# Kernel optimization log

Measured on AMD Instinct MI355X. Metric: run time of the kernel, lower is better.

## Reference

```python
import jax, jax.numpy as jnp
import numpy as np

B, LQ, LK = 4, 1024, 2048
DQ, DK, DV, D = 1024, 512, 512, 1024
H = 16
HD = D // H
EPS = 1e-5


def setup_inputs() -> dict:
    key = jax.random.key(0)
    ks = jax.random.split(key, 12)
    s = lambda fan: 1.0 / np.sqrt(fan)
    return {
        "query": jax.random.normal(ks[0], (B, LQ, DQ), jnp.float32),
        "key": jax.random.normal(ks[1], (B, LK, DK), jnp.float32),
        "value": jax.random.normal(ks[2], (B, LK, DV), jnp.float32),
        "key_padding_mask": jnp.ones((B, LK), jnp.int32),
        "Wq": jax.random.normal(ks[3], (DQ, D), jnp.float32) * s(DQ),
        "bq": jnp.zeros((D,), jnp.float32),
        "Wk": jax.random.normal(ks[4], (DK, D), jnp.float32) * s(DK),
        "bk": jnp.zeros((D,), jnp.float32),
        "Wv": jax.random.normal(ks[5], (DV, D), jnp.float32) * s(DV),
        "bv": jnp.zeros((D,), jnp.float32),
        "Wo": jax.random.normal(ks[6], (D, D), jnp.float32) * s(D),
        "bo": jnp.zeros((D,), jnp.float32),
        "ln_g": jnp.ones((D,), jnp.float32),
        "ln_b": jnp.zeros((D,), jnp.float32),
    }


def _layer_norm(x, g, b):
    mu = jnp.mean(x, axis=-1, keepdims=True)
    var = jnp.mean(jnp.square(x - mu), axis=-1, keepdims=True)
    return (x - mu) * jax.lax.rsqrt(var + EPS) * g + b


def reference(query, key, value, key_padding_mask, Wq, bq, Wk, bk, Wv, bv, Wo, bo, ln_g, ln_b):
    residual = query
    qn = _layer_norm(query, ln_g, ln_b)
    # projections -> [B, L, H, HD]
    q = (qn @ Wq + bq).reshape(B, LQ, H, HD)
    k = (key @ Wk + bk).reshape(B, LK, H, HD)
    v = (value @ Wv + bv).reshape(B, LK, H, HD)
    scale = HD ** -0.5
    # scores [B, H, Lq, Lk]
    scores = jnp.einsum("bqhd,bkhd->bhqk", q, k) * scale
    mask = (key_padding_mask != 0)[:, None, None, :]  # True = keep
    scores = jnp.where(mask, scores, -jnp.inf)
    attn = jax.nn.softmax(scores, axis=-1)
    # dropout is identity in eval mode
    ctx = jnp.einsum("bhqk,bkhd->bqhd", attn, v).reshape(B, LQ, D)
    out = ctx @ Wo + bo
    return out + residual
```

## Files before the change

### kernel.cpp

```cpp
#include <hip/hip_runtime.h>
#include <hip/hip_bf16.h>
#include <stdint.h>

#define Bn 4
#define LQ 1024
#define LK 2048
#define Dm 1024
#define Hn 16
#define HD 64

typedef __attribute__((ext_vector_type(4))) float f32x4;
typedef __attribute__((ext_vector_type(16))) float f32x16;
typedef __attribute__((ext_vector_type(8))) short bf16x8;

__device__ __forceinline__ ushort f2bf(float f) {
  union { float f; uint32_t u; } v; v.f = f;
  uint32_t r = v.u + 0x7FFF + ((v.u >> 16) & 1);
  return (ushort)(r >> 16);
}

__device__ __forceinline__ uint32_t cvt_pk_bf16(float lo, float hi) {
  uint32_t r;
  asm("v_cvt_pk_bf16_f32 %0, %1, %2" : "=v"(r) : "v"(lo), "v"(hi));
  return r;
}

__device__ __forceinline__ float exp2v(float x) {
  float r;
  asm("v_exp_f32 %0, %1" : "=v"(r) : "v"(x));
  return r;
}

__device__ __forceinline__ void gload16(const void* g, void* lds) {
  __builtin_amdgcn_global_load_lds(
      (const __attribute__((address_space(1))) void*)g,
      (__attribute__((address_space(3))) void*)lds, 16, 0, 0);
}

__device__ __forceinline__ void wait_vm0_barrier() {
  asm volatile("s_waitcnt vmcnt(0)" ::: "memory");
  __builtin_amdgcn_s_barrier();
}

__device__ __forceinline__ void wait_all_barrier() {
  asm volatile("s_waitcnt vmcnt(0) lgkmcnt(0)" ::: "memory");
  __builtin_amdgcn_s_barrier();
}

__global__ __launch_bounds__(256) void transpose_cast_kernel(
    const float* __restrict__ W, ushort* __restrict__ Wt, int K, int N) {
  __shared__ float tile[64][65];
  int k0 = blockIdx.x * 64, n0 = blockIdx.y * 64;
  int tx = threadIdx.x & 63, ty = threadIdx.x >> 6;
#pragma unroll
  for (int i = 0; i < 16; ++i) {
    int r = ty + i * 4;
    tile[r][tx] = W[(size_t)(k0 + r) * N + n0 + tx];
  }
  __syncthreads();
#pragma unroll
  for (int i = 0; i < 16; ++i) {
    int r = ty + i * 4;
    Wt[(size_t)(n0 + r) * K + k0 + tx] = f2bf(tile[tx][r]);
  }
}

__global__ __launch_bounds__(256) void cast_bf16_kernel(
    const float4* __restrict__ in, ushort4* __restrict__ out, int n4) {
  int i = blockIdx.x * blockDim.x + threadIdx.x;
  int stride = gridDim.x * blockDim.x;
  for (; i < n4; i += stride) {
    float4 v = in[i];
    out[i] = make_ushort4(f2bf(v.x), f2bf(v.y), f2bf(v.z), f2bf(v.w));
  }
}

__global__ __launch_bounds__(256) void ln_kernel(
    const float* __restrict__ x, const float* __restrict__ g,
    const float* __restrict__ b, ushort* __restrict__ y) {
  int row = blockIdx.x;
  const float4* xr = (const float4*)(x + (size_t)row * 1024);
  float4 v = xr[threadIdx.x];
  float s1 = v.x + v.y + v.z + v.w;
  float s2 = v.x * v.x + v.y * v.y + v.z * v.z + v.w * v.w;
#pragma unroll
  for (int off = 32; off > 0; off >>= 1) {
    s1 += __shfl_down(s1, off);
    s2 += __shfl_down(s2, off);
  }
  __shared__ float r1[4], r2[4];
  int w = threadIdx.x >> 6, lane = threadIdx.x & 63;
  if (lane == 0) { r1[w] = s1; r2[w] = s2; }
  __syncthreads();
  s1 = r1[0] + r1[1] + r1[2] + r1[3];
  s2 = r2[0] + r2[1] + r2[2] + r2[3];
  float mu = s1 * (1.0f / 1024.0f);
  float var = s2 * (1.0f / 1024.0f) - mu * mu;
  float rstd = rsqrtf(var + 1e-5f);
  float4 gv = ((const float4*)g)[threadIdx.x];
  float4 bv = ((const float4*)b)[threadIdx.x];
  ushort4 o;
  o.x = f2bf((v.x - mu) * rstd * gv.x + bv.x);
  o.y = f2bf((v.y - mu) * rstd * gv.y + bv.y);
  o.z = f2bf((v.z - mu) * rstd * gv.z + bv.z);
  o.w = f2bf((v.w - mu) * rstd * gv.w + bv.w);
  ((ushort4*)(y + (size_t)row * 1024))[threadIdx.x] = o;
}

__global__ __launch_bounds__(256) void qkv_gemm_kernel(
    const ushort* __restrict__ qn, const ushort* __restrict__ WqT,
    const float* __restrict__ bq, ushort* __restrict__ Qb,
    const ushort* __restrict__ keyb, const ushort* __restrict__ WkT,
    const float* __restrict__ bk, ushort* __restrict__ Kb,
    const ushort* __restrict__ valb, const ushort* __restrict__ WvT,
    const float* __restrict__ bv, ushort* __restrict__ Vt, float qscale) {
  __shared__ ushort As[2][128 * 64];
  __shared__ ushort Bs[2][128 * 64];

  int o = blockIdx.x;
  int logical = (o & 7) * 160 + (o >> 3);
  const ushort* A; const ushort* Bt; const float* bias; ushort* out;
  int M, K, bx, by, epi; float osc = 1.0f;
  if (logical < 256) {
    A = qn; Bt = WqT; bias = bq; out = Qb; M = 4096; K = 1024; epi = 0;
    osc = qscale; bx = logical & 7; by = logical >> 3;
  } else if (logical < 768) {
    int i = logical - 256;
    A = keyb; Bt = WkT; bias = bk; out = Kb; M = 8192; K = 512; epi = 0;
    bx = i & 7; by = i >> 3;
  } else {
    int i = logical - 768;
    A = valb; Bt = WvT; bias = bv; out = Vt; M = 8192; K = 512; epi = 1;
    bx = i & 7; by = i >> 3;
  }
  const int N = 1024;
  const int m0 = by * 128, n0 = bx * 128;

  const int t = threadIdx.x;
  const int lane = t & 63;
  const int w = t >> 6;
  const int wm = w >> 1, wn = w & 1;
  const int l31 = lane & 31, hl = lane >> 5;

  f32x16 acc[2][2] = {};

  const ushort* Ap[4];
  const ushort* Bp[4];
#pragma unroll
  for (int i = 0; i < 4; ++i) {
    int c = t + i * 256;
    int r = c >> 3, x = ((c & 7) ^ (r & 7)) * 8;
    Ap[i] = A + (size_t)(m0 + r) * K + x;
    Bp[i] = Bt + (size_t)(n0 + r) * K + x;
  }

  auto stage = [&](int buf, int kt) {
#pragma unroll
    for (int i = 0; i < 4; ++i) {
      gload16(Ap[i] + kt, (char*)As[buf] + (t + i * 256) * 16);
      gload16(Bp[i] + kt, (char*)Bs[buf] + (t + i * 256) * 16);
    }
  };

  stage(0, 0);
  wait_vm0_barrier();

  int cur = 0;
  for (int kt = 0; kt < K; kt += 64) {
    if (kt + 64 < K) stage(cur ^ 1, kt + 64);
    bf16x8 af[2][4], bfr[2][4];
#pragma unroll
    for (int m = 0; m < 2; ++m) {
      int row = wm * 64 + m * 32 + l31;
      const char* ar = (const char*)As[cur] + row * 128;
      int rs = row & 7;
#pragma unroll
      for (int kc = 0; kc < 4; ++kc)
        af[m][kc] = *(const bf16x8*)(ar + ((kc * 2 + hl) ^ rs) * 16);
    }
#pragma unroll
    for (int n = 0; n < 2; ++n) {
      int row = wn * 64 + n * 32 + l31;
      const char* br = (const char*)Bs[cur] + row * 128;
      int rs = row & 7;
#pragma unroll
      for (int kc = 0; kc < 4; ++kc)
        bfr[n][kc] = *(const bf16x8*)(br + ((kc * 2 + hl) ^ rs) * 16);
    }
#pragma unroll
    for (int kc = 0; kc < 4; ++kc)
#pragma unroll
      for (int m = 0; m < 2; ++m)
#pragma unroll
        for (int n = 0; n < 2; ++n)
          acc[m][n] = __builtin_amdgcn_mfma_f32_32x32x16_bf16(af[m][kc], bfr[n][kc], acc[m][n], 0, 0, 0);
    wait_vm0_barrier();
    cur ^= 1;
  }

  float bias_v[2];
#pragma unroll
  for (int n = 0; n < 2; ++n) bias_v[n] = bias[n0 + wn * 64 + n * 32 + l31];

#pragma unroll
  for (int m = 0; m < 2; ++m) {
    int rbase = m0 + wm * 64 + m * 32 + hl * 4;
#pragma unroll
    for (int n = 0; n < 2; ++n) {
      int col = n0 + wn * 64 + n * 32 + l31;
#pragma unroll
      for (int rq = 0; rq < 4; ++rq) {
        int row0 = rbase + rq * 8;
        if (epi == 1) {
          int bb = row0 >> 11;
          int key = row0 & 2047;
          int h = col >> 6, hd = col & 63;
          ushort4 pk;
          pk.x = f2bf(acc[m][n][rq * 4 + 0] + bias_v[n]);
          pk.y = f2bf(acc[m][n][rq * 4 + 1] + bias_v[n]);
          pk.z = f2bf(acc[m][n][rq * 4 + 2] + bias_v[n]);
          pk.w = f2bf(acc[m][n][rq * 4 + 3] + bias_v[n]);
          *(ushort4*)(out + ((size_t)((bb * 16 + h) * 64 + hd)) * 2048 + key) = pk;
        } else {
#pragma unroll
          for (int j = 0; j < 4; ++j) {
            int row = row0 + j;
            float v = (acc[m][n][rq * 4 + j] + bias_v[n]) * osc;
            out[(size_t)row * N + col] = f2bf(v);
          }
        }
      }
    }
  }
}

__global__ __launch_bounds__(256) void oproj_gemm_kernel(
    const ushort* __restrict__ A, const ushort* __restrict__ Bt,
    const float* __restrict__ bias, float* __restrict__ Cout,
    const float* __restrict__ residual, int M, int N, int K) {
  __shared__ ushort As[2][128 * 64];
  __shared__ ushort Bs[2][128 * 64];
  const int t = threadIdx.x;
  const int lane = t & 63;
  const int w = t >> 6;
  const int wm = w >> 1, wn = w & 1;
  const int m0 = blockIdx.y * 128, n0 = blockIdx.x * 128;
  const int l31 = lane & 31, hl = lane >> 5;

  f32x16 acc[2][2] = {};

  const ushort* Ap[4];
  const ushort* Bp[4];
#pragma unroll
  for (int i = 0; i < 4; ++i) {
    int c = t + i * 256;
    int r = c >> 3, x = ((c & 7) ^ (r & 7)) * 8;
    Ap[i] = A + (size_t)(m0 + r) * K + x;
    Bp[i] = Bt + (size_t)(n0 + r) * K + x;
  }

  auto stage = [&](int buf, int kt) {
#pragma unroll
    for (int i = 0; i < 4; ++i) {
      gload16(Ap[i] + kt, (char*)As[buf] + (t + i * 256) * 16);
      gload16(Bp[i] + kt, (char*)Bs[buf] + (t + i * 256) * 16);
    }
  };

  stage(0, 0);
  wait_vm0_barrier();

  int cur = 0;
  for (int kt = 0; kt < K; kt += 64) {
    if (kt + 64 < K) stage(cur ^ 1, kt + 64);
    bf16x8 af[2][4], bfr[2][4];
#pragma unroll
    for (int m = 0; m < 2; ++m) {
      int row = wm * 64 + m * 32 + l31;
      const char* ar = (const char*)As[cur] + row * 128;
      int rs = row & 7;
#pragma unroll
      for (int kc = 0; kc < 4; ++kc)
        af[m][kc] = *(const bf16x8*)(ar + ((kc * 2 + hl) ^ rs) * 16);
    }
#pragma unroll
    for (int n = 0; n < 2; ++n) {
      int row = wn * 64 + n * 32 + l31;
      const char* br = (const char*)Bs[cur] + row * 128;
      int rs = row & 7;
#pragma unroll
      for (int kc = 0; kc < 4; ++kc)
        bfr[n][kc] = *(const bf16x8*)(br + ((kc * 2 + hl) ^ rs) * 16);
    }
#pragma unroll
    for (int kc = 0; kc < 4; ++kc)
#pragma unroll
      for (int m = 0; m < 2; ++m)
#pragma unroll
        for (int n = 0; n < 2; ++n)
          acc[m][n] = __builtin_amdgcn_mfma_f32_32x32x16_bf16(af[m][kc], bfr[n][kc], acc[m][n], 0, 0, 0);
    wait_vm0_barrier();
    cur ^= 1;
  }

  float bias_v[2];
#pragma unroll
  for (int n = 0; n < 2; ++n) bias_v[n] = bias[n0 + wn * 64 + n * 32 + l31];

#pragma unroll
  for (int m = 0; m < 2; ++m) {
    int rbase = m0 + wm * 64 + m * 32 + hl * 4;
#pragma unroll
    for (int n = 0; n < 2; ++n) {
      int col = n0 + wn * 64 + n * 32 + l31;
#pragma unroll
      for (int rq = 0; rq < 4; ++rq) {
        int row0 = rbase + rq * 8;
#pragma unroll
        for (int j = 0; j < 4; ++j) {
          size_t idx = (size_t)(row0 + j) * N + col;
          Cout[idx] = acc[m][n][rq * 4 + j] + bias_v[n] + residual[idx];
        }
      }
    }
  }
}

__global__ __launch_bounds__(256) void attn_kernel(
    const ushort* __restrict__ Qb, const ushort* __restrict__ Kb,
    const ushort* __restrict__ Vt, const int* __restrict__ mask,
    ushort* __restrict__ ctx) {
  __shared__ __align__(16) char smem[128 + 2 * 16384];
  int* tilevalid = (int*)smem;
  char* KsBase = smem + 128;
  char* VsBase = smem + 128 + 16384;

  const int t = threadIdx.x, lane = t & 63, w = t >> 6;
  const int l31 = lane & 31, hl = lane >> 5;
  int o = blockIdx.x;
  int logical = (o & 7) * 64 + (o >> 3);
  const int b = logical >> 7;
  const int hh = (logical >> 3) & 15;
  const int q0 = (logical & 7) * 128;
  const int* maskp = mask + b * 2048;

  const int cA = t, cB = t + 256;
  const int rA = cA >> 3, rB = cB >> 3;
  const int xA = ((cA & 7) ^ (rA & 7)) * 8, xB = ((cB & 7) ^ (rB & 7)) * 8;
  const ushort* kpA = Kb + ((size_t)(b * 2048 + rA)) * 1024 + hh * 64 + xA;
  const ushort* kpB = Kb + ((size_t)(b * 2048 + rB)) * 1024 + hh * 64 + xB;
  const ushort* vpA = Vt + ((size_t)((b * 16 + hh) * 64 + rA)) * 2048 + xA;
  const ushort* vpB = Vt + ((size_t)((b * 16 + hh) * 64 + rB)) * 2048 + xB;

  auto stageKV = [&](int buf) {
    char* kd = KsBase + buf * 8192;
    char* vd = VsBase + buf * 8192;
    gload16(kpA, kd + cA * 16);
    gload16(kpB, kd + cB * 16);
    gload16(vpA, vd + cA * 16);
    gload16(vpB, vd + cB * 16);
  };

  if (t < 32) tilevalid[t] = 1;
  __syncthreads();
  stageKV(0);
  {
    const int* mp = maskp + t * 8;
    int ok = 1;
#pragma unroll
    for (int j = 0; j < 8; ++j) ok &= (mp[j] != 0) ? 1 : 0;
    atomicAnd(&tilevalid[t >> 3], ok);
  }

  bf16x8 qf[4];
  {
    int qrow = q0 + w * 32 + l31;
    const ushort* qp = Qb + ((size_t)(b * 1024 + qrow)) * 1024 + hh * 64 + hl * 8;
    qf[0] = *(const bf16x8*)(qp);
    qf[1] = *(const bf16x8*)(qp + 16);
    qf[2] = *(const bf16x8*)(qp + 32);
    qf[3] = *(const bf16x8*)(qp + 48);
  }

  const int rs = l31 & 7;
  int lo[2][2][4];
#pragma unroll
  for (int bu = 0; bu < 2; ++bu)
#pragma unroll
    for (int r2 = 0; r2 < 2; ++r2)
#pragma unroll
      for (int kc = 0; kc < 4; ++kc)
        lo[bu][r2][kc] = 128 + bu * 8192 + (r2 * 32 + l31) * 128 + (((kc * 2 + hl) ^ rs) * 16);

  f32x16 o_acc[2] = {};
  float m_run = -1e30f, l_run = 0.0f;

  wait_all_barrier();

  auto body = [&](const int CUR, int TILE) __attribute__((always_inline)) {
    if (TILE + 1 < 32) {
      kpA += 64 * 1024; kpB += 64 * 1024; vpA += 64; vpB += 64;
      stageKV(CUR ^ 1);
    }

    f32x16 sacc[2] = {};
    __builtin_amdgcn_s_setprio(1);
#pragma unroll
    for (int kb = 0; kb < 2; ++kb)
#pragma unroll
      for (int kc = 0; kc < 4; ++kc) {
        bf16x8 kf = *(const bf16x8*)(smem + lo[CUR][kb][kc]);
        sacc[kb] = __builtin_amdgcn_mfma_f32_32x32x16_bf16(kf, qf[kc], sacc[kb], 0, 0, 0);
      }
    __builtin_amdgcn_s_setprio(0);

    int allv = __builtin_amdgcn_readfirstlane(tilevalid[TILE]);
    if (!allv) {
      const int* mrow = maskp + TILE * 64 + 4 * hl;
#pragma unroll
      for (int kb = 0; kb < 2; ++kb)
#pragma unroll
        for (int rq = 0; rq < 4; ++rq) {
          int4 mv = *(const int4*)(mrow + kb * 32 + rq * 8);
          sacc[kb][rq * 4 + 0] = mv.x ? sacc[kb][rq * 4 + 0] : -1e30f;
          sacc[kb][rq * 4 + 1] = mv.y ? sacc[kb][rq * 4 + 1] : -1e30f;
          sacc[kb][rq * 4 + 2] = mv.z ? sacc[kb][rq * 4 + 2] : -1e30f;
          sacc[kb][rq * 4 + 3] = mv.w ? sacc[kb][rq * 4 + 3] : -1e30f;
        }
    }

    float tm = fmaxf(sacc[0][0], sacc[0][1]);
#pragma unroll
    for (int r = 2; r < 16; r += 2) tm = fmaxf(fmaxf(tm, sacc[0][r]), sacc[0][r + 1]);
#pragma unroll
    for (int r = 0; r < 16; r += 2) tm = fmaxf(fmaxf(tm, sacc[1][r]), sacc[1][r + 1]);
    {
      float s1 = tm, s2 = tm;
      asm("v_permlane32_swap_b32 %0, %1" : "+v"(s1), "+v"(s2));
      tm = fmaxf(tm, hl ? s1 : s2);
    }

    if (__any(tm - m_run > 11.5f)) {
      float mn = fmaxf(m_run, tm);
      float al = exp2v(m_run - mn);
      m_run = mn;
      l_run *= al;
#pragma unroll
      for (int df = 0; df < 2; ++df)
#pragma unroll
        for (int r = 0; r < 16; ++r) o_acc[df][r] *= al;
    }

    float psA = 0.0f, psB = 0.0f;
    uint32_t cpk[2][8];
#pragma unroll
    for (int kb = 0; kb < 2; ++kb)
#pragma unroll
      for (int rr = 0; rr < 8; ++rr) {
        float pa = exp2v(sacc[kb][2 * rr] - m_run);
        float pb = exp2v(sacc[kb][2 * rr + 1] - m_run);
        psA += pa; psB += pb;
        cpk[kb][rr] = cvt_pk_bf16(pa, pb);
      }
    float psum = psA + psB;
    {
      float s1 = psum, s2 = psum;
      asm("v_permlane32_swap_b32 %0, %1" : "+v"(s1), "+v"(s2));
      psum += hl ? s1 : s2;
    }
    l_run += psum;

    __builtin_amdgcn_s_setprio(1);
#pragma unroll
    for (int ks = 0; ks < 4; ++ks) {
      const int kb = ks >> 1, ci = (ks & 1) * 4;
      uint32_t a0 = cpk[kb][ci],     b0 = cpk[kb][ci + 2];
      uint32_t a1 = cpk[kb][ci + 1], b1 = cpk[kb][ci + 3];
      asm("v_permlane32_swap_b32 %0, %1" : "+v"(a0), "+v"(b0));
      asm("v_permlane32_swap_b32 %0, %1" : "+v"(a1), "+v"(b1));
      union { uint32_t u[4]; bf16x8 v; } pb_;
      pb_.u[0] = a0; pb_.u[1] = a1; pb_.u[2] = b0; pb_.u[3] = b1;
#pragma unroll
      for (int df = 0; df < 2; ++df) {
        bf16x8 vf = *(const bf16x8*)(smem + lo[CUR][df][ks] + 16384);
        o_acc[df] = __builtin_amdgcn_mfma_f32_32x32x16_bf16(vf, pb_.v, o_acc[df], 0, 0, 0);
      }
    }
    __builtin_amdgcn_s_setprio(0);

    wait_vm0_barrier();
  };

  for (int tile = 0; tile < 32; tile += 2) {
    body(0, tile);
    body(1, tile + 1);
  }

  float inv = l_run > 0.0f ? 1.0f / l_run : 0.0f;
  char* ob = KsBase + w * 4096;
#pragma unroll
  for (int df = 0; df < 2; ++df)
#pragma unroll
    for (int rq = 0; rq < 4; ++rq) {
      ushort4 pk;
      pk.x = f2bf(o_acc[df][rq * 4 + 0] * inv);
      pk.y = f2bf(o_acc[df][rq * 4 + 1] * inv);
      pk.z = f2bf(o_acc[df][rq * 4 + 2] * inv);
      pk.w = f2bf(o_acc[df][rq * 4 + 3] * inv);
      *(ushort4*)(ob + l31 * 128 + (((df * 4 + rq) ^ (l31 & 7)) * 16) + hl * 8) = pk;
    }
  asm volatile("s_waitcnt lgkmcnt(0)" ::: "memory");
#pragma unroll
  for (int i = 0; i < 4; ++i) {
    int q = (lane >> 3) + i * 8;
    int ch = lane & 7;
    uint4 v = *(const uint4*)(ob + q * 128 + ((ch ^ (q & 7)) * 16));
    int qrow = q0 + w * 32 + q;
    *(uint4*)(ctx + ((size_t)(b * 1024 + qrow)) * 1024 + hh * 64 + ch * 8) = v;
  }
}

extern "C" void kernel_launch(void* const* d_in, const int* in_sizes, int n_in,
                              void* d_out, int out_size, void* d_ws, size_t ws_size,
                              hipStream_t stream) {
  const float* query = (const float*)d_in[0];
  const float* key   = (const float*)d_in[1];
  const float* value = (const float*)d_in[2];
  const int*   mask  = (const int*)d_in[3];
  const float* Wq = (const float*)d_in[4];
  const float* bq = (const float*)d_in[5];
  const float* Wk = (const float*)d_in[6];
  const float* bk = (const float*)d_in[7];
  const float* Wv = (const float*)d_in[8];
  const float* bv = (const float*)d_in[9];
  const float* Wo = (const float*)d_in[10];
  const float* bo = (const float*)d_in[11];
  const float* ln_g = (const float*)d_in[12];
  const float* ln_b = (const float*)d_in[13];
  float* out = (float*)d_out;

  char* p = (char*)d_ws;
  auto alloc = [&](size_t elems) { ushort* r = (ushort*)p; p += elems * 2; return r; };
  ushort* WqT  = alloc((size_t)1024 * 1024);
  ushort* WkT  = alloc((size_t)1024 * 512);
  ushort* WvT  = alloc((size_t)1024 * 512);
  ushort* WoT  = alloc((size_t)1024 * 1024);
  ushort* qn   = alloc((size_t)4096 * 1024);
  ushort* keyb = alloc((size_t)8192 * 512);
  ushort* valb = alloc((size_t)8192 * 512);
  ushort* Qb   = alloc((size_t)4096 * 1024);
  ushort* Kb   = alloc((size_t)8192 * 1024);
  ushort* Vt   = alloc((size_t)8192 * 1024);
  ushort* ctx  = alloc((size_t)4096 * 1024);
  (void)ws_size; (void)in_sizes; (void)n_in; (void)out_size;

  const float QSCALE = 0.125f * 1.44269504f;

  dim3 blk(256);
  transpose_cast_kernel<<<dim3(16, 16), blk, 0, stream>>>(Wq, WqT, 1024, 1024);
  transpose_cast_kernel<<<dim3(8, 16),  blk, 0, stream>>>(Wk, WkT, 512, 1024);
  transpose_cast_kernel<<<dim3(8, 16),  blk, 0, stream>>>(Wv, WvT, 512, 1024);
  transpose_cast_kernel<<<dim3(16, 16), blk, 0, stream>>>(Wo, WoT, 1024, 1024);
  cast_bf16_kernel<<<dim3(1024), blk, 0, stream>>>((const float4*)key,   (ushort4*)keyb, (8192 * 512) / 4);
  cast_bf16_kernel<<<dim3(1024), blk, 0, stream>>>((const float4*)value, (ushort4*)valb, (8192 * 512) / 4);
  ln_kernel<<<dim3(4096), blk, 0, stream>>>(query, ln_g, ln_b, qn);

  qkv_gemm_kernel<<<dim3(1280), blk, 0, stream>>>(
      qn, WqT, bq, Qb, keyb, WkT, bk, Kb, valb, WvT, bv, Vt, QSCALE);

  attn_kernel<<<dim3(512), blk, 0, stream>>>(Qb, Kb, Vt, mask, ctx);

  oproj_gemm_kernel<<<dim3(8, 32), blk, 0, stream>>>(ctx, WoT, bo, out, query, 4096, 1024, 1024);
}
```

Measured before the change: 165.9 us.

## Use 8 waves per GEMM block and overlap next-tile loads with compute

Both the QKV and output-projection GEMM kernels move from 4 to 8 waves per 128x128 tile, so each wave computes a 64x32 sub-tile with half the accumulators and half the global loads per thread. The K loop now issues the next stage's loads and waits only for the previous stage (vmcnt(4)) before the barrier. The end-of-iteration barrier waits only on LDS reads. The aim is more latency hiding through extra waves and overlap of memory with MFMA work. In exchange, the A fragments are read from LDS by twice as many waves.

```diff
diff --git a/kernel.cpp b/kernel.cpp
--- a/kernel.cpp
+++ b/kernel.cpp
@@ -44,6 +44,11 @@
 
 __device__ __forceinline__ void wait_all_barrier() {
   asm volatile("s_waitcnt vmcnt(0) lgkmcnt(0)" ::: "memory");
+  __builtin_amdgcn_s_barrier();
+}
+
+__device__ __forceinline__ void wait_lgkm0_barrier() {
+  asm volatile("s_waitcnt lgkmcnt(0)" ::: "memory");
   __builtin_amdgcn_s_barrier();
 }
 
@@ -107,7 +112,7 @@
   ((ushort4*)(y + (size_t)row * 1024))[threadIdx.x] = o;
 }
 
-__global__ __launch_bounds__(256) void qkv_gemm_kernel(
+__global__ __launch_bounds__(512) void qkv_gemm_kernel(
     const ushort* __restrict__ qn, const ushort* __restrict__ WqT,
     const float* __restrict__ bq, ushort* __restrict__ Qb,
     const ushort* __restrict__ keyb, const ushort* __restrict__ WkT,
@@ -120,17 +125,17 @@
   int o = blockIdx.x;
   int logical = (o & 7) * 160 + (o >> 3);
   const ushort* A; const ushort* Bt; const float* bias; ushort* out;
-  int M, K, bx, by, epi; float osc = 1.0f;
+  int K, bx, by, epi; float osc = 1.0f;
   if (logical < 256) {
-    A = qn; Bt = WqT; bias = bq; out = Qb; M = 4096; K = 1024; epi = 0;
+    A = qn; Bt = WqT; bias = bq; out = Qb; K = 1024; epi = 0;
     osc = qscale; bx = logical & 7; by = logical >> 3;
   } else if (logical < 768) {
     int i = logical - 256;
-    A = keyb; Bt = WkT; bias = bk; out = Kb; M = 8192; K = 512; epi = 0;
+    A = keyb; Bt = WkT; bias = bk; out = Kb; K = 512; epi = 0;
     bx = i & 7; by = i >> 3;
   } else {
     int i = logical - 768;
-    A = valb; Bt = WvT; bias = bv; out = Vt; M = 8192; K = 512; epi = 1;
+    A = valb; Bt = WvT; bias = bv; out = Vt; K = 512; epi = 1;
     bx = i & 7; by = i >> 3;
   }
   const int N = 1024;
@@ -139,36 +144,41 @@
   const int t = threadIdx.x;
   const int lane = t & 63;
   const int w = t >> 6;
-  const int wm = w >> 1, wn = w & 1;
+  const int wm = w >> 2, wn = w & 3;
   const int l31 = lane & 31, hl = lane >> 5;
 
-  f32x16 acc[2][2] = {};
-
-  const ushort* Ap[4];
-  const ushort* Bp[4];
-#pragma unroll
-  for (int i = 0; i < 4; ++i) {
-    int c = t + i * 256;
+  f32x16 acc[2] = {};
+
+  const ushort* Ap[2];
+  const ushort* Bp[2];
+#pragma unroll
+  for (int i = 0; i < 2; ++i) {
+    int c = t + i * 512;
     int r = c >> 3, x = ((c & 7) ^ (r & 7)) * 8;
     Ap[i] = A + (size_t)(m0 + r) * K + x;
     Bp[i] = Bt + (size_t)(n0 + r) * K + x;
   }
 
   auto stage = [&](int buf, int kt) {
-#pragma unroll
-    for (int i = 0; i < 4; ++i) {
-      gload16(Ap[i] + kt, (char*)As[buf] + (t + i * 256) * 16);
-      gload16(Bp[i] + kt, (char*)Bs[buf] + (t + i * 256) * 16);
-    }
+    gload16(Ap[0] + kt, (char*)As[buf] + (size_t)t * 16);
+    gload16(Ap[1] + kt, (char*)As[buf] + (size_t)(t + 512) * 16);
+    gload16(Bp[0] + kt, (char*)Bs[buf] + (size_t)t * 16);
+    gload16(Bp[1] + kt, (char*)Bs[buf] + (size_t)(t + 512) * 16);
   };
 
   stage(0, 0);
-  wait_vm0_barrier();
 
   int cur = 0;
   for (int kt = 0; kt < K; kt += 64) {
-    if (kt + 64 < K) stage(cur ^ 1, kt + 64);
-    bf16x8 af[2][4], bfr[2][4];
+    if (kt + 64 < K) {
+      stage(cur ^ 1, kt + 64);
+      asm volatile("s_waitcnt vmcnt(4)" ::: "memory");
+    } else {
+      asm volatile("s_waitcnt vmcnt(0)" ::: "memory");
+    }
+    __builtin_amdgcn_s_barrier();
+
+    bf16x8 af[2][4], bfr[4];
 #pragma unroll
     for (int m = 0; m < 2; ++m) {
       int row = wm * 64 + m * 32 + l31;
@@ -178,63 +188,56 @@
       for (int kc = 0; kc < 4; ++kc)
         af[m][kc] = *(const bf16x8*)(ar + ((kc * 2 + hl) ^ rs) * 16);
     }
-#pragma unroll
-    for (int n = 0; n < 2; ++n) {
-      int row = wn * 64 + n * 32 + l31;
+    {
+      int row = wn * 32 + l31;
       const char* br = (const char*)Bs[cur] + row * 128;
       int rs = row & 7;
 #pragma unroll
       for (int kc = 0; kc < 4; ++kc)
-        bfr[n][kc] = *(const bf16x8*)(br + ((kc * 2 + hl) ^ rs) * 16);
+        bfr[kc] = *(const bf16x8*)(br + ((kc * 2 + hl) ^ rs) * 16);
     }
 #pragma unroll
     for (int kc = 0; kc < 4; ++kc)
 #pragma unroll
       for (int m = 0; m < 2; ++m)
-#pragma unroll
-        for (int n = 0; n < 2; ++n)
-          acc[m][n] = __builtin_amdgcn_mfma_f32_32x32x16_bf16(af[m][kc], bfr[n][kc], acc[m][n], 0, 0, 0);
-    wait_vm0_barrier();
+        acc[m] = __builtin_amdgcn_mfma_f32_32x32x16_bf16(af[m][kc], bfr[kc], acc[m], 0, 0, 0);
+
+    wait_lgkm0_barrier();
     cur ^= 1;
   }
 
-  float bias_v[2];
-#pragma unroll
-  for (int n = 0; n < 2; ++n) bias_v[n] = bias[n0 + wn * 64 + n * 32 + l31];
+  const int col = n0 + wn * 32 + l31;
+  const float bias_v = bias[col];
 
 #pragma unroll
   for (int m = 0; m < 2; ++m) {
     int rbase = m0 + wm * 64 + m * 32 + hl * 4;
 #pragma unroll
-    for (int n = 0; n < 2; ++n) {
-      int col = n0 + wn * 64 + n * 32 + l31;
-#pragma unroll
-      for (int rq = 0; rq < 4; ++rq) {
-        int row0 = rbase + rq * 8;
-        if (epi == 1) {
-          int bb = row0 >> 11;
-          int key = row0 & 2047;
-          int h = col >> 6, hd = col & 63;
-          ushort4 pk;
-          pk.x = f2bf(acc[m][n][rq * 4 + 0] + bias_v[n]);
-          pk.y = f2bf(acc[m][n][rq * 4 + 1] + bias_v[n]);
-          pk.z = f2bf(acc[m][n][rq * 4 + 2] + bias_v[n]);
-          pk.w = f2bf(acc[m][n][rq * 4 + 3] + bias_v[n]);
-          *(ushort4*)(out + ((size_t)((bb * 16 + h) * 64 + hd)) * 2048 + key) = pk;
-        } else {
-#pragma unroll
-          for (int j = 0; j < 4; ++j) {
-            int row = row0 + j;
-            float v = (acc[m][n][rq * 4 + j] + bias_v[n]) * osc;
-            out[(size_t)row * N + col] = f2bf(v);
-          }
+    for (int rq = 0; rq < 4; ++rq) {
+      int row0 = rbase + rq * 8;
+      if (epi == 1) {
+        int bb = row0 >> 11;
+        int key = row0 & 2047;
+        int h = col >> 6, hd = col & 63;
+        ushort4 pk;
+        pk.x = f2bf(acc[m][rq * 4 + 0] + bias_v);
+        pk.y = f2bf(acc[m][rq * 4 + 1] + bias_v);
+        pk.z = f2bf(acc[m][rq * 4 + 2] + bias_v);
+        pk.w = f2bf(acc[m][rq * 4 + 3] + bias_v);
+        *(ushort4*)(out + ((size_t)((bb * 16 + h) * 64 + hd)) * 2048 + key) = pk;
+      } else {
+#pragma unroll
+        for (int j = 0; j < 4; ++j) {
+          int row = row0 + j;
+          float v = (acc[m][rq * 4 + j] + bias_v) * osc;
+          out[(size_t)row * N + col] = f2bf(v);
         }
       }
     }
   }
 }
 
-__global__ __launch_bounds__(256) void oproj_gemm_kernel(
+__global__ __launch_bounds__(512) void oproj_gemm_kernel(
     const ushort* __restrict__ A, const ushort* __restrict__ Bt,
     const float* __restrict__ bias, float* __restrict__ Cout,
     const float* __restrict__ residual, int M, int N, int K) {
@@ -243,37 +246,42 @@
   const int t = threadIdx.x;
   const int lane = t & 63;
   const int w = t >> 6;
-  const int wm = w >> 1, wn = w & 1;
+  const int wm = w >> 2, wn = w & 3;
   const int m0 = blockIdx.y * 128, n0 = blockIdx.x * 128;
   const int l31 = lane & 31, hl = lane >> 5;
 
-  f32x16 acc[2][2] = {};
-
-  const ushort* Ap[4];
-  const ushort* Bp[4];
-#pragma unroll
-  for (int i = 0; i < 4; ++i) {
-    int c = t + i * 256;
+  f32x16 acc[2] = {};
+
+  const ushort* Ap[2];
+  const ushort* Bp[2];
+#pragma unroll
+  for (int i = 0; i < 2; ++i) {
+    int c = t + i * 512;
     int r = c >> 3, x = ((c & 7) ^ (r & 7)) * 8;
     Ap[i] = A + (size_t)(m0 + r) * K + x;
     Bp[i] = Bt + (size_t)(n0 + r) * K + x;
   }
 
   auto stage = [&](int buf, int kt) {
-#pragma unroll
-    for (int i = 0; i < 4; ++i) {
-      gload16(Ap[i] + kt, (char*)As[buf] + (t + i * 256) * 16);
-      gload16(Bp[i] + kt, (char*)Bs[buf] + (t + i * 256) * 16);
-    }
+    gload16(Ap[0] + kt, (char*)As[buf] + (size_t)t * 16);
+    gload16(Ap[1] + kt, (char*)As[buf] + (size_t)(t + 512) * 16);
+    gload16(Bp[0] + kt, (char*)Bs[buf] + (size_t)t * 16);
+    gload16(Bp[1] + kt, (char*)Bs[buf] + (size_t)(t + 512) * 16);
   };
 
   stage(0, 0);
-  wait_vm0_barrier();
 
   int cur = 0;
   for (int kt = 0; kt < K; kt += 64) {
-    if (kt + 64 < K) stage(cur ^ 1, kt + 64);
-    bf16x8 af[2][4], bfr[2][4];
+    if (kt + 64 < K) {
+      stage(cur ^ 1, kt + 64);
+      asm volatile("s_waitcnt vmcnt(4)" ::: "memory");
+    } else {
+      asm volatile("s_waitcnt vmcnt(0)" ::: "memory");
+    }
+    __builtin_amdgcn_s_barrier();
+
+    bf16x8 af[2][4], bfr[4];
 #pragma unroll
     for (int m = 0; m < 2; ++m) {
       int row = wm * 64 + m * 32 + l31;
@@ -283,44 +291,37 @@
       for (int kc = 0; kc < 4; ++kc)
         af[m][kc] = *(const bf16x8*)(ar + ((kc * 2 + hl) ^ rs) * 16);
     }
-#pragma unroll
-    for (int n = 0; n < 2; ++n) {
-      int row = wn * 64 + n * 32 + l31;
+    {
+      int row = wn * 32 + l31;
       const char* br = (const char*)Bs[cur] + row * 128;
       int rs = row & 7;
 #pragma unroll
       for (int kc = 0; kc < 4; ++kc)
-        bfr[n][kc] = *(const bf16x8*)(br + ((kc * 2 + hl) ^ rs) * 16);
+        bfr[kc] = *(const bf16x8*)(br + ((kc * 2 + hl) ^ rs) * 16);
     }
 #pragma unroll
     for (int kc = 0; kc < 4; ++kc)
 #pragma unroll
       for (int m = 0; m < 2; ++m)
-#pragma unroll
-        for (int n = 0; n < 2; ++n)
-          acc[m][n] = __builtin_amdgcn_mfma_f32_32x32x16_bf16(af[m][kc], bfr[n][kc], acc[m][n], 0, 0, 0);
-    wait_vm0_barrier();
+        acc[m] = __builtin_amdgcn_mfma_f32_32x32x16_bf16(af[m][kc], bfr[kc], acc[m], 0, 0, 0);
+
+    wait_lgkm0_barrier();
     cur ^= 1;
   }
 
-  float bias_v[2];
-#pragma unroll
-  for (int n = 0; n < 2; ++n) bias_v[n] = bias[n0 + wn * 64 + n * 32 + l31];
+  const int col = n0 + wn * 32 + l31;
+  const float bias_v = bias[col];
 
 #pragma unroll
   for (int m = 0; m < 2; ++m) {
     int rbase = m0 + wm * 64 + m * 32 + hl * 4;
 #pragma unroll
-    for (int n = 0; n < 2; ++n) {
-      int col = n0 + wn * 64 + n * 32 + l31;
-#pragma unroll
-      for (int rq = 0; rq < 4; ++rq) {
-        int row0 = rbase + rq * 8;
-#pragma unroll
-        for (int j = 0; j < 4; ++j) {
-          size_t idx = (size_t)(row0 + j) * N + col;
-          Cout[idx] = acc[m][n][rq * 4 + j] + bias_v[n] + residual[idx];
-        }
+    for (int rq = 0; rq < 4; ++rq) {
+      int row0 = rbase + rq * 8;
+#pragma unroll
+      for (int j = 0; j < 4; ++j) {
+        size_t idx = (size_t)(row0 + j) * N + col;
+        Cout[idx] = acc[m][rq * 4 + j] + bias_v + residual[idx];
       }
     }
   }
@@ -557,6 +558,7 @@
   const float QSCALE = 0.125f * 1.44269504f;
 
   dim3 blk(256);
+  dim3 blk5(512);
   transpose_cast_kernel<<<dim3(16, 16), blk, 0, stream>>>(Wq, WqT, 1024, 1024);
   transpose_cast_kernel<<<dim3(8, 16),  blk, 0, stream>>>(Wk, WkT, 512, 1024);
   transpose_cast_kernel<<<dim3(8, 16),  blk, 0, stream>>>(Wv, WvT, 512, 1024);
@@ -565,10 +567,10 @@
   cast_bf16_kernel<<<dim3(1024), blk, 0, stream>>>((const float4*)value, (ushort4*)valb, (8192 * 512) / 4);
   ln_kernel<<<dim3(4096), blk, 0, stream>>>(query, ln_g, ln_b, qn);
 
-  qkv_gemm_kernel<<<dim3(1280), blk, 0, stream>>>(
+  qkv_gemm_kernel<<<dim3(1280), blk5, 0, stream>>>(
       qn, WqT, bq, Qb, keyb, WkT, bk, Kb, valb, WvT, bv, Vt, QSCALE);
 
   attn_kernel<<<dim3(512), blk, 0, stream>>>(Qb, Kb, Vt, mask, ctx);
 
-  oproj_gemm_kernel<<<dim3(8, 32), blk, 0, stream>>>(ctx, WoT, bo, out, query, 4096, 1024, 1024);
-}
+  oproj_gemm_kernel<<<dim3(8, 32), blk5, 0, stream>>>(ctx, WoT, bo, out, query, 4096, 1024, 1024);
+}
```

After: 162.2 us. 1.02x faster.

## Merge prep kernel launches and overlap GEMM prefetch with partial vmcnt waits

Applied to the files above, without the earlier changes.

Fuses the four weight transpose-cast launches into one grid and the two key/value cast launches into one, cutting launch overhead and the small-grid tails between them. In both GEMM main loops, the full vmcnt(0) wait at the end of each iteration is replaced by a partial vmcnt(8) wait issued after the next stage's loads, plus an lgkmcnt barrier after the MFMAs. This lets next-tile global-to-LDS loads stay in flight while the current tile is computed. The waits rely on the exact count of outstanding loads per stage (8 per thread), so they are fragile if staging changes.

```diff
diff --git a/kernel.cpp b/kernel.cpp
--- a/kernel.cpp
+++ b/kernel.cpp
@@ -47,10 +47,19 @@
   __builtin_amdgcn_s_barrier();
 }
 
-__global__ __launch_bounds__(256) void transpose_cast_kernel(
-    const float* __restrict__ W, ushort* __restrict__ Wt, int K, int N) {
+__global__ __launch_bounds__(256) void transpose4_kernel(
+    const float* __restrict__ Wq, ushort* __restrict__ WqT,
+    const float* __restrict__ Wk, ushort* __restrict__ WkT,
+    const float* __restrict__ Wv, ushort* __restrict__ WvT,
+    const float* __restrict__ Wo, ushort* __restrict__ WoT) {
   __shared__ float tile[64][65];
-  int k0 = blockIdx.x * 64, n0 = blockIdx.y * 64;
+  int id = blockIdx.x;
+  const float* W; ushort* Wt; int K, N, kx, ny;
+  if (id < 256)      { W = Wq; Wt = WqT; K = 1024; N = 1024; kx = id & 15; ny = id >> 4; }
+  else if (id < 384) { int i = id - 256; W = Wk; Wt = WkT; K = 512; N = 1024; kx = i & 7; ny = i >> 3; }
+  else if (id < 512) { int i = id - 384; W = Wv; Wt = WvT; K = 512; N = 1024; kx = i & 7; ny = i >> 3; }
+  else               { int i = id - 512; W = Wo; Wt = WoT; K = 1024; N = 1024; kx = i & 15; ny = i >> 4; }
+  int k0 = kx * 64, n0 = ny * 64;
   int tx = threadIdx.x & 63, ty = threadIdx.x >> 6;
 #pragma unroll
   for (int i = 0; i < 16; ++i) {
@@ -65,13 +74,16 @@
   }
 }
 
-__global__ __launch_bounds__(256) void cast_bf16_kernel(
-    const float4* __restrict__ in, ushort4* __restrict__ out, int n4) {
-  int i = blockIdx.x * blockDim.x + threadIdx.x;
-  int stride = gridDim.x * blockDim.x;
-  for (; i < n4; i += stride) {
-    float4 v = in[i];
-    out[i] = make_ushort4(f2bf(v.x), f2bf(v.y), f2bf(v.z), f2bf(v.w));
+__global__ __launch_bounds__(256) void cast2_kernel(
+    const float4* __restrict__ k4, ushort4* __restrict__ kb,
+    const float4* __restrict__ v4, ushort4* __restrict__ vb) {
+  const int n4 = (8192 * 512) / 4;
+  int i = blockIdx.x * 256 + threadIdx.x;
+  int stride = gridDim.x * 256;
+  for (; i < 2 * n4; i += stride) {
+    float4 v = (i < n4) ? k4[i] : v4[i - n4];
+    ushort4 o = make_ushort4(f2bf(v.x), f2bf(v.y), f2bf(v.z), f2bf(v.w));
+    if (i < n4) kb[i] = o; else vb[i - n4] = o;
   }
 }
 
@@ -120,17 +132,17 @@
   int o = blockIdx.x;
   int logical = (o & 7) * 160 + (o >> 3);
   const ushort* A; const ushort* Bt; const float* bias; ushort* out;
-  int M, K, bx, by, epi; float osc = 1.0f;
+  int K, bx, by, epi; float osc = 1.0f;
   if (logical < 256) {
-    A = qn; Bt = WqT; bias = bq; out = Qb; M = 4096; K = 1024; epi = 0;
+    A = qn; Bt = WqT; bias = bq; out = Qb; K = 1024; epi = 0;
     osc = qscale; bx = logical & 7; by = logical >> 3;
   } else if (logical < 768) {
     int i = logical - 256;
-    A = keyb; Bt = WkT; bias = bk; out = Kb; M = 8192; K = 512; epi = 0;
+    A = keyb; Bt = WkT; bias = bk; out = Kb; K = 512; epi = 0;
     bx = i & 7; by = i >> 3;
   } else {
     int i = logical - 768;
-    A = valb; Bt = WvT; bias = bv; out = Vt; M = 8192; K = 512; epi = 1;
+    A = valb; Bt = WvT; bias = bv; out = Vt; K = 512; epi = 1;
     bx = i & 7; by = i >> 3;
   }
   const int N = 1024;
@@ -163,11 +175,17 @@
   };
 
   stage(0, 0);
-  wait_vm0_barrier();
 
   int cur = 0;
   for (int kt = 0; kt < K; kt += 64) {
-    if (kt + 64 < K) stage(cur ^ 1, kt + 64);
+    if (kt + 64 < K) {
+      stage(cur ^ 1, kt + 64);
+      asm volatile("s_waitcnt vmcnt(8)" ::: "memory");
+    } else {
+      asm volatile("s_waitcnt vmcnt(0)" ::: "memory");
+    }
+    __builtin_amdgcn_s_barrier();
+
     bf16x8 af[2][4], bfr[2][4];
 #pragma unroll
     for (int m = 0; m < 2; ++m) {
@@ -194,7 +212,9 @@
 #pragma unroll
         for (int n = 0; n < 2; ++n)
           acc[m][n] = __builtin_amdgcn_mfma_f32_32x32x16_bf16(af[m][kc], bfr[n][kc], acc[m][n], 0, 0, 0);
-    wait_vm0_barrier();
+
+    asm volatile("s_waitcnt lgkmcnt(0)" ::: "memory");
+    __builtin_amdgcn_s_barrier();
     cur ^= 1;
   }
 
@@ -268,11 +288,17 @@
   };
 
   stage(0, 0);
-  wait_vm0_barrier();
 
   int cur = 0;
   for (int kt = 0; kt < K; kt += 64) {
-    if (kt + 64 < K) stage(cur ^ 1, kt + 64);
+    if (kt + 64 < K) {
+      stage(cur ^ 1, kt + 64);
+      asm volatile("s_waitcnt vmcnt(8)" ::: "memory");
+    } else {
+      asm volatile("s_waitcnt vmcnt(0)" ::: "memory");
+    }
+    __builtin_amdgcn_s_barrier();
+
     bf16x8 af[2][4], bfr[2][4];
 #pragma unroll
     for (int m = 0; m < 2; ++m) {
@@ -299,7 +325,9 @@
 #pragma unroll
         for (int n = 0; n < 2; ++n)
           acc[m][n] = __builtin_amdgcn_mfma_f32_32x32x16_bf16(af[m][kc], bfr[n][kc], acc[m][n], 0, 0, 0);
-    wait_vm0_barrier();
+
+    asm volatile("s_waitcnt lgkmcnt(0)" ::: "memory");
+    __builtin_amdgcn_s_barrier();
     cur ^= 1;
   }
 
@@ -557,12 +585,9 @@
   const float QSCALE = 0.125f * 1.44269504f;
 
   dim3 blk(256);
-  transpose_cast_kernel<<<dim3(16, 16), blk, 0, stream>>>(Wq, WqT, 1024, 1024);
-  transpose_cast_kernel<<<dim3(8, 16),  blk, 0, stream>>>(Wk, WkT, 512, 1024);
-  transpose_cast_kernel<<<dim3(8, 16),  blk, 0, stream>>>(Wv, WvT, 512, 1024);
-  transpose_cast_kernel<<<dim3(16, 16), blk, 0, stream>>>(Wo, WoT, 1024, 1024);
-  cast_bf16_kernel<<<dim3(1024), blk, 0, stream>>>((const float4*)key,   (ushort4*)keyb, (8192 * 512) / 4);
-  cast_bf16_kernel<<<dim3(1024), blk, 0, stream>>>((const float4*)value, (ushort4*)valb, (8192 * 512) / 4);
+  transpose4_kernel<<<dim3(768), blk, 0, stream>>>(Wq, WqT, Wk, WkT, Wv, WvT, Wo, WoT);
+  cast2_kernel<<<dim3(2048), blk, 0, stream>>>(
+      (const float4*)key, (ushort4*)keyb, (const float4*)value, (ushort4*)valb);
   ln_kernel<<<dim3(4096), blk, 0, stream>>>(query, ln_g, ln_b, qn);
 
   qkv_gemm_kernel<<<dim3(1280), blk, 0, stream>>>(
```

Result: faster. 159.1 us (-4.1%).
